# Performance work log

Hardware: AMD Instinct MI355X
Metric: run time of the kernel (lower is better)

Reference implementation:

```python
import jax, jax.numpy as jnp
import numpy as np

N_NODES = 100000
N_EDGES = 1600000
D_IN = 128
D_OUT = 5


def setup_inputs() -> dict:
    key = jax.random.key(0)
    k1, k2, k3, k4, k5 = jax.random.split(key, 5)
    x = jax.random.normal(k1, (N_NODES, D_IN), dtype=jnp.float32)
    edge_index = jax.random.randint(k2, (2, N_EDGES), 0, N_NODES, dtype=jnp.int64)
    scale = 1.0 / np.sqrt(D_IN)
    W_l = jax.random.normal(k3, (D_OUT, D_IN), dtype=jnp.float32) * scale
    b_l = jax.random.normal(k4, (D_OUT,), dtype=jnp.float32) * scale
    W_r = jax.random.normal(k5, (D_OUT, D_IN), dtype=jnp.float32) * scale
    return {"x": x, "edge_index": edge_index, "W_l": W_l, "b_l": b_l, "W_r": W_r}


def reference(x, edge_index, W_l, b_l, W_r):
    # PyG SAGEConv with aggr='mean', root_weight=True:
    # out_i = mean_{j: (j->i) in E} x_j @ W_l^T + b_l + x_i @ W_r^T
    n = x.shape[0]
    src = edge_index[0]
    dst = edge_index[1]
    msgs = x[src]  # [E, D_in] gather (irregular access)
    agg_sum = jax.ops.segment_sum(msgs, dst, num_segments=n)  # [N, D_in]
    deg = jax.ops.segment_sum(jnp.ones(src.shape, dtype=x.dtype), dst, num_segments=n)
    agg_mean = agg_sum / jnp.maximum(deg, 1.0)[:, None]  # zero-degree nodes -> 0
    out = agg_mean @ W_l.T + b_l + x @ W_r.T  # [N, D_out]
    return out
```

## Files before the change

kernel.cpp:

```cpp
#include <hip/hip_runtime.h>
#include <hip/hip_bf16.h>


#define N_NODES 100000
#define N_EDGES 1600000
#define D_IN 128

#define HL_STRIDE 8
#define N_PAD 100352

#define B_NODES 196
#define N_BUCKETS 512
#define CAP 3840

#define SC_EPT 8
#define SC_EPB (256 * SC_EPT)
#define SC_GRID ((N_EDGES + SC_EPB - 1) / SC_EPB)

#define NPG 8
#define PROJ_NPB (16 * NPG)
#define PROJ_BLOCKS ((N_NODES + PROJ_NPB - 1) / PROJ_NPB)
#define FUSED_GRID (PROJ_BLOCKS + SC_GRID)

#define FXS 262144.0f
#define FXB 16777216u
#define FXBF 16777216.0f
#define INV_FXS (1.0f / 262144.0f)

typedef unsigned long long u64;
typedef unsigned int u32;

__global__ __launch_bounds__(256, 4) void proj_scatter_kernel(
    const float* __restrict__ x,
    const float* __restrict__ Wl,
    const float* __restrict__ Wr,
    float* __restrict__ hl,
    float* __restrict__ hr,
    const int* __restrict__ ei,
    u32* __restrict__ sorted,
    int* __restrict__ cursor)
{
    const int tid = threadIdx.x;

    if (blockIdx.x < PROJ_BLOCKS) {
        const int g = tid >> 4;
        const int k = tid & 15;

        float4 wv[10][2];
#pragma unroll
        for (int o = 0; o < 10; ++o) {
            const float* w = (o < 5 ? Wl + o * D_IN : Wr + (o - 5) * D_IN) + k * 8;
            wv[o][0] = ((const float4*)w)[0];
            wv[o][1] = ((const float4*)w)[1];
        }

        const int node0 = blockIdx.x * PROJ_NPB + g * NPG;

#pragma unroll
        for (int it = 0; it < NPG; ++it) {
            const int node = min(node0 + it, N_NODES - 1);

            const float4* xr = (const float4*)(x + (size_t)node * D_IN + k * 8);
            float4 x0 = xr[0];
            float4 x1 = xr[1];

            float s[10];
#pragma unroll
            for (int o = 0; o < 10; ++o) {
                s[o] = x0.x * wv[o][0].x + x0.y * wv[o][0].y
                     + x0.z * wv[o][0].z + x0.w * wv[o][0].w
                     + x1.x * wv[o][1].x + x1.y * wv[o][1].y
                     + x1.z * wv[o][1].z + x1.w * wv[o][1].w;
            }

#pragma unroll
            for (int o = 0; o < 10; ++o) {
                s[o] += __shfl_xor(s[o], 8, 64);
                s[o] += __shfl_xor(s[o], 4, 64);
                s[o] += __shfl_xor(s[o], 2, 64);
                s[o] += __shfl_xor(s[o], 1, 64);
            }

            if (k == 0) {
                float* pl = hl + (size_t)node * HL_STRIDE;
                *(float4*)pl = make_float4(s[0], s[1], s[2], s[3]);
                pl[4] = s[4];
                float* pr = hr + (size_t)node * HL_STRIDE;
                *(float4*)pr = make_float4(s[5], s[6], s[7], s[8]);
                pr[4] = s[9];
            }
        }
    } else {
        __shared__ int hist[N_BUCKETS];
        __shared__ int basepos[N_BUCKETS];

        for (int i = tid; i < N_BUCKETS; i += 256) hist[i] = 0;
        __syncthreads();

        const int blk = blockIdx.x - PROJ_BLOCKS;
        const int e0  = blk * SC_EPB + tid * SC_EPT;

        int srcv[SC_EPT], dstv[SC_EPT], slot[SC_EPT];
        bool valid[SC_EPT];

        if (e0 + SC_EPT <= N_EDGES) {
            const int4* s4 = (const int4*)(ei + e0);
            const int4* d4 = (const int4*)(ei + N_EDGES + e0);
            int4 sa = s4[0], sb = s4[1], da = d4[0], db = d4[1];
            srcv[0]=sa.x; srcv[1]=sa.y; srcv[2]=sa.z; srcv[3]=sa.w;
            srcv[4]=sb.x; srcv[5]=sb.y; srcv[6]=sb.z; srcv[7]=sb.w;
            dstv[0]=da.x; dstv[1]=da.y; dstv[2]=da.z; dstv[3]=da.w;
            dstv[4]=db.x; dstv[5]=db.y; dstv[6]=db.z; dstv[7]=db.w;
#pragma unroll
            for (int q = 0; q < SC_EPT; ++q) valid[q] = true;
        } else {
#pragma unroll
            for (int q = 0; q < SC_EPT; ++q) {
                int e = e0 + q;
                valid[q] = (e < N_EDGES);
                srcv[q] = valid[q] ? ei[e] : 0;
                dstv[q] = valid[q] ? ei[N_EDGES + e] : 0;
            }
        }

#pragma unroll
        for (int q = 0; q < SC_EPT; ++q) {
            if (valid[q]) {
                unsigned b = (unsigned)dstv[q] / 196u;
                slot[q] = atomicAdd(&hist[b], 1);
            }
        }
        __syncthreads();

        for (int b = tid; b < N_BUCKETS; b += 256) {
            int c = hist[b];
            if (c > 0) basepos[b] = atomicAdd(&cursor[b], c);
        }
        __syncthreads();

#pragma unroll
        for (int q = 0; q < SC_EPT; ++q) {
            if (valid[q]) {
                unsigned b = (unsigned)dstv[q] / 196u;
                unsigned r = (unsigned)dstv[q] - b * 196u;
                sorted[(size_t)b * CAP + basepos[b] + slot[q]] =
                    (r << 17) | (unsigned)srcv[q];
            }
        }
    }
}

__global__ __launch_bounds__(512) void agg_kernel(
    const u32* __restrict__ sorted,
    const int* __restrict__ cursor,
    const float* __restrict__ hl,
    const float* __restrict__ hr,
    const float* __restrict__ bias,
    float* __restrict__ out)
{
    __shared__ u64 acc[B_NODES * 3];

    const int b   = blockIdx.x;
    const int tid = threadIdx.x;

    for (int i = tid; i < B_NODES * 3; i += 512) acc[i] = 0ull;
    __syncthreads();

    const int cnt = cursor[b];
    const u32* sp = sorted + (size_t)b * CAP;
    const int nvec = cnt >> 2;

#define EMIT(hh, ee, rr)                                                     \
    {                                                                        \
        u32 f0 = __float2uint_rn(fmaf((hh).x, FXS, FXBF));                   \
        u32 f1 = __float2uint_rn(fmaf((hh).y, FXS, FXBF));                   \
        u32 f2 = __float2uint_rn(fmaf((hh).z, FXS, FXBF));                   \
        u32 f3 = __float2uint_rn(fmaf((hh).w, FXS, FXBF));                   \
        u32 f4 = __float2uint_rn(fmaf((ee),   FXS, FXBF));                   \
        u64* a = acc + (rr) * 3;                                             \
        atomicAdd(&a[0], ((u64)f1 << 32) | f0);                              \
        atomicAdd(&a[1], ((u64)f3 << 32) | f2);                              \
        atomicAdd(&a[2], ((u64)f4 << 32) | 1u);                              \
    }

    for (int it = tid; it < nvec; it += 512) {
        uint4 v = ((const uint4*)sp)[it];
        int s0 = (int)(v.x & 0x1FFFFu), r0 = (int)(v.x >> 17);
        int s1 = (int)(v.y & 0x1FFFFu), r1 = (int)(v.y >> 17);
        int s2 = (int)(v.z & 0x1FFFFu), r2 = (int)(v.z >> 17);
        int s3 = (int)(v.w & 0x1FFFFu), r3 = (int)(v.w >> 17);

        const float* p0 = hl + (size_t)s0 * HL_STRIDE;
        const float* p1 = hl + (size_t)s1 * HL_STRIDE;
        const float* p2 = hl + (size_t)s2 * HL_STRIDE;
        const float* p3 = hl + (size_t)s3 * HL_STRIDE;
        float4 h0 = *(const float4*)p0; float e0 = p0[4];
        float4 h1 = *(const float4*)p1; float e1 = p1[4];
        float4 h2 = *(const float4*)p2; float e2 = p2[4];
        float4 h3 = *(const float4*)p3; float e3 = p3[4];

        EMIT(h0, e0, r0) EMIT(h1, e1, r1) EMIT(h2, e2, r2) EMIT(h3, e3, r3)
    }
    for (int i = (nvec << 2) + tid; i < cnt; i += 512) {
        u32 v = sp[i];
        int src = (int)(v & 0x1FFFFu);
        int r   = (int)(v >> 17);
        const float* p = hl + (size_t)src * HL_STRIDE;
        float4 h = *(const float4*)p;
        float  e = p[4];
        EMIT(h, e, r)
    }
#undef EMIT
    __syncthreads();

    const int nodebase = b * B_NODES;
    for (int n = tid; n < B_NODES; n += 512) {
        int node = nodebase + n;
        if (node >= N_NODES) continue;
        u64 w0 = acc[n * 3 + 0];
        u64 w1 = acc[n * 3 + 1];
        u64 w2 = acc[n * 3 + 2];
        u32 deg = (u32)(w2 & 0xFFFFFFFFu);
        u32 db  = deg * FXB;
        int i0 = (int)((u32)(w0 & 0xFFFFFFFFu) - db);
        int i1 = (int)((u32)(w0 >> 32)         - db);
        int i2 = (int)((u32)(w1 & 0xFFFFFFFFu) - db);
        int i3 = (int)((u32)(w1 >> 32)         - db);
        int i4 = (int)((u32)(w2 >> 32)         - db);

        float rec = INV_FXS / fmaxf((float)deg, 1.0f);
        const float* h = hr + (size_t)node * HL_STRIDE;
        float* o = out + (size_t)node * 5;
        o[0] = (float)i0 * rec + bias[0] + h[0];
        o[1] = (float)i1 * rec + bias[1] + h[1];
        o[2] = (float)i2 * rec + bias[2] + h[2];
        o[3] = (float)i3 * rec + bias[3] + h[3];
        o[4] = (float)i4 * rec + bias[4] + h[4];
    }
}

extern "C" void kernel_launch(void* const* d_in, const int* in_sizes, int n_in,
                              void* d_out, int out_size, void* d_ws, size_t ws_size,
                              hipStream_t stream) {
    const float* x    = (const float*)d_in[0];
    const int*   ei   = (const int*)d_in[1];
    const float* Wl   = (const float*)d_in[2];
    const float* bl   = (const float*)d_in[3];
    const float* Wr   = (const float*)d_in[4];
    float*       out  = (float*)d_out;

    float* hl     = (float*)d_ws;
    float* hr     = hl + (size_t)N_PAD * HL_STRIDE;
    u32*   sorted = (u32*)(hr + (size_t)N_PAD * HL_STRIDE);
    int*   cursor = (int*)(sorted + (size_t)N_BUCKETS * CAP);

    hipMemsetAsync(cursor, 0, N_BUCKETS * sizeof(int), stream);

    proj_scatter_kernel<<<FUSED_GRID, 256, 0, stream>>>(
        x, Wl, Wr, hl, hr, ei, sorted, cursor);

    agg_kernel<<<N_BUCKETS, 512, 0, stream>>>(sorted, cursor, hl, hr, bl, out);
}
```

Before: 130.9 us.

## Scatter larger edge chunks per block with two-pass histogram to cut global atomics

Each scatter block now handles 16384 edges instead of 2048. It does a histogram pass over destination buckets, then a second pass that re-reads the edges and assigns slots, so each block issues one global cursor atomic per bucket over a much larger batch. The scatter blocks are also placed before the projection blocks in the grid so the latency-bound scatter work is dispatched first. In exchange the edge arrays are read twice, there are far fewer scatter blocks and so less parallelism in that phase, and more shared-memory atomic contention per block.

Measured after the change: 140.3 us. 1.07x slower.

```diff
diff --git a/kernel.cpp b/kernel.cpp
--- a/kernel.cpp
+++ b/kernel.cpp
@@ -13,14 +13,14 @@
 #define N_BUCKETS 512
 #define CAP 3840
 
-#define SC_EPT 8
-#define SC_EPB (256 * SC_EPT)
+#define SC_EPB 16384
 #define SC_GRID ((N_EDGES + SC_EPB - 1) / SC_EPB)
+#define SC_CHUNKS (SC_EPB / 1024)
 
 #define NPG 8
 #define PROJ_NPB (16 * NPG)
 #define PROJ_BLOCKS ((N_NODES + PROJ_NPB - 1) / PROJ_NPB)
-#define FUSED_GRID (PROJ_BLOCKS + SC_GRID)
+#define FUSED_GRID (SC_GRID + PROJ_BLOCKS)
 
 #define FXS 262144.0f
 #define FXB 16777216u
@@ -42,7 +42,57 @@
 {
     const int tid = threadIdx.x;
 
-    if (blockIdx.x < PROJ_BLOCKS) {
+    if (blockIdx.x < SC_GRID) {
+        __shared__ int hist[N_BUCKETS];
+        __shared__ int basepos[N_BUCKETS];
+
+        for (int i = tid; i < N_BUCKETS; i += 256) hist[i] = 0;
+        __syncthreads();
+
+        const int e0 = blockIdx.x * SC_EPB;
+
+#pragma unroll
+        for (int c = 0; c < SC_CHUNKS; ++c) {
+            int e = e0 + (c << 10) + (tid << 2);
+            if (e < N_EDGES) {
+                int4 d4 = *(const int4*)(ei + N_EDGES + e);
+                atomicAdd(&hist[(unsigned)d4.x / 196u], 1);
+                atomicAdd(&hist[(unsigned)d4.y / 196u], 1);
+                atomicAdd(&hist[(unsigned)d4.z / 196u], 1);
+                atomicAdd(&hist[(unsigned)d4.w / 196u], 1);
+            }
+        }
+        __syncthreads();
+
+        for (int b = tid; b < N_BUCKETS; b += 256) {
+            int c = hist[b];
+            if (c > 0) basepos[b] = atomicAdd(&cursor[b], c);
+        }
+        __syncthreads();
+
+        for (int i = tid; i < N_BUCKETS; i += 256) hist[i] = 0;
+        __syncthreads();
+
+#pragma unroll
+        for (int c = 0; c < SC_CHUNKS; ++c) {
+            int e = e0 + (c << 10) + (tid << 2);
+            if (e < N_EDGES) {
+                int4 s4 = *(const int4*)(ei + e);
+                int4 d4 = *(const int4*)(ei + N_EDGES + e);
+                int sv[4] = { s4.x, s4.y, s4.z, s4.w };
+                int dv[4] = { d4.x, d4.y, d4.z, d4.w };
+#pragma unroll
+                for (int q = 0; q < 4; ++q) {
+                    unsigned b = (unsigned)dv[q] / 196u;
+                    unsigned r = (unsigned)dv[q] - b * 196u;
+                    int slot = atomicAdd(&hist[b], 1);
+                    sorted[(size_t)b * CAP + basepos[b] + slot] =
+                        (r << 17) | (unsigned)sv[q];
+                }
+            }
+        }
+    } else {
+        const int pblk = blockIdx.x - SC_GRID;
         const int g = tid >> 4;
         const int k = tid & 15;
 
@@ -54,7 +104,7 @@
             wv[o][1] = ((const float4*)w)[1];
         }
 
-        const int node0 = blockIdx.x * PROJ_NPB + g * NPG;
+        const int node0 = pblk * PROJ_NPB + g * NPG;
 
 #pragma unroll
         for (int it = 0; it < NPG; ++it) {
@@ -88,63 +138,6 @@
                 float* pr = hr + (size_t)node * HL_STRIDE;
                 *(float4*)pr = make_float4(s[5], s[6], s[7], s[8]);
                 pr[4] = s[9];
-            }
-        }
-    } else {
-        __shared__ int hist[N_BUCKETS];
-        __shared__ int basepos[N_BUCKETS];
-
-        for (int i = tid; i < N_BUCKETS; i += 256) hist[i] = 0;
-        __syncthreads();
-
-        const int blk = blockIdx.x - PROJ_BLOCKS;
-        const int e0  = blk * SC_EPB + tid * SC_EPT;
-
-        int srcv[SC_EPT], dstv[SC_EPT], slot[SC_EPT];
-        bool valid[SC_EPT];
-
-        if (e0 + SC_EPT <= N_EDGES) {
-            const int4* s4 = (const int4*)(ei + e0);
-            const int4* d4 = (const int4*)(ei + N_EDGES + e0);
-            int4 sa = s4[0], sb = s4[1], da = d4[0], db = d4[1];
-            srcv[0]=sa.x; srcv[1]=sa.y; srcv[2]=sa.z; srcv[3]=sa.w;
-            srcv[4]=sb.x; srcv[5]=sb.y; srcv[6]=sb.z; srcv[7]=sb.w;
-            dstv[0]=da.x; dstv[1]=da.y; dstv[2]=da.z; dstv[3]=da.w;
-            dstv[4]=db.x; dstv[5]=db.y; dstv[6]=db.z; dstv[7]=db.w;
-#pragma unroll
-            for (int q = 0; q < SC_EPT; ++q) valid[q] = true;
-        } else {
-#pragma unroll
-            for (int q = 0; q < SC_EPT; ++q) {
-                int e = e0 + q;
-                valid[q] = (e < N_EDGES);
-                srcv[q] = valid[q] ? ei[e] : 0;
-                dstv[q] = valid[q] ? ei[N_EDGES + e] : 0;
-            }
-        }
-
-#pragma unroll
-        for (int q = 0; q < SC_EPT; ++q) {
-            if (valid[q]) {
-                unsigned b = (unsigned)dstv[q] / 196u;
-                slot[q] = atomicAdd(&hist[b], 1);
-            }
-        }
-        __syncthreads();
-
-        for (int b = tid; b < N_BUCKETS; b += 256) {
-            int c = hist[b];
-            if (c > 0) basepos[b] = atomicAdd(&cursor[b], c);
-        }
-        __syncthreads();
-
-#pragma unroll
-        for (int q = 0; q < SC_EPT; ++q) {
-            if (valid[q]) {
-                unsigned b = (unsigned)dstv[q] / 196u;
-                unsigned r = (unsigned)dstv[q] - b * 196u;
-                sorted[(size_t)b * CAP + basepos[b] + slot[q]] =
-                    (r << 17) | (unsigned)srcv[q];
             }
         }
     }
```

## Compute node projections with bf16 MFMA tiles instead of FP32 dot products

Applied to the files above, without the earlier changes.

Replaces the per-node FP32 dot-product-plus-shuffle-reduction projection with a 16x16x32 bf16 MFMA: each wave handles a 16-node tile, x rows and the 10 weight rows are converted to bf16 and accumulated over 4 K-steps. This removes the shuffle reductions and most VALU work in the projection part of the fused kernel. It trades precision (bf16 inputs), and the tile count assumes N_NODES is divisible by 16.

Result: no change. 132.2 us (+1.0%).

```diff
diff --git a/kernel.cpp b/kernel.cpp
--- a/kernel.cpp
+++ b/kernel.cpp
@@ -17,9 +17,8 @@
 #define SC_EPB (256 * SC_EPT)
 #define SC_GRID ((N_EDGES + SC_EPB - 1) / SC_EPB)
 
-#define NPG 8
-#define PROJ_NPB (16 * NPG)
-#define PROJ_BLOCKS ((N_NODES + PROJ_NPB - 1) / PROJ_NPB)
+#define N_TILES (N_NODES / 16)
+#define PROJ_BLOCKS ((N_TILES + 3) / 4)
 #define FUSED_GRID (PROJ_BLOCKS + SC_GRID)
 
 #define FXS 262144.0f
@@ -29,6 +28,23 @@
 
 typedef unsigned long long u64;
 typedef unsigned int u32;
+typedef __attribute__((ext_vector_type(8))) short bf16x8;
+typedef __attribute__((ext_vector_type(4))) float f32x4;
+
+__device__ __forceinline__ u32 pack_bf16(float lo, float hi) {
+    u32 a = (__float_as_uint(lo) + 0x8000u) >> 16;
+    u32 b = (__float_as_uint(hi) + 0x8000u) & 0xFFFF0000u;
+    return a | b;
+}
+
+__device__ __forceinline__ bf16x8 pack8(float4 v0, float4 v1) {
+    union { u32 w[4]; bf16x8 v; } u;
+    u.w[0] = pack_bf16(v0.x, v0.y);
+    u.w[1] = pack_bf16(v0.z, v0.w);
+    u.w[2] = pack_bf16(v1.x, v1.y);
+    u.w[3] = pack_bf16(v1.z, v1.w);
+    return u.v;
+}
 
 __global__ __launch_bounds__(256, 4) void proj_scatter_kernel(
     const float* __restrict__ x,
@@ -43,51 +59,44 @@
     const int tid = threadIdx.x;
 
     if (blockIdx.x < PROJ_BLOCKS) {
-        const int g = tid >> 4;
-        const int k = tid & 15;
-
-        float4 wv[10][2];
-#pragma unroll
-        for (int o = 0; o < 10; ++o) {
-            const float* w = (o < 5 ? Wl + o * D_IN : Wr + (o - 5) * D_IN) + k * 8;
-            wv[o][0] = ((const float4*)w)[0];
-            wv[o][1] = ((const float4*)w)[1];
-        }
-
-        const int node0 = blockIdx.x * PROJ_NPB + g * NPG;
-
-#pragma unroll
-        for (int it = 0; it < NPG; ++it) {
-            const int node = min(node0 + it, N_NODES - 1);
-
-            const float4* xr = (const float4*)(x + (size_t)node * D_IN + k * 8);
-            float4 x0 = xr[0];
-            float4 x1 = xr[1];
-
-            float s[10];
-#pragma unroll
-            for (int o = 0; o < 10; ++o) {
-                s[o] = x0.x * wv[o][0].x + x0.y * wv[o][0].y
-                     + x0.z * wv[o][0].z + x0.w * wv[o][0].w
-                     + x1.x * wv[o][1].x + x1.y * wv[o][1].y
-                     + x1.z * wv[o][1].z + x1.w * wv[o][1].w;
-            }
-
-#pragma unroll
-            for (int o = 0; o < 10; ++o) {
-                s[o] += __shfl_xor(s[o], 8, 64);
-                s[o] += __shfl_xor(s[o], 4, 64);
-                s[o] += __shfl_xor(s[o], 2, 64);
-                s[o] += __shfl_xor(s[o], 1, 64);
-            }
-
-            if (k == 0) {
-                float* pl = hl + (size_t)node * HL_STRIDE;
-                *(float4*)pl = make_float4(s[0], s[1], s[2], s[3]);
-                pl[4] = s[4];
-                float* pr = hr + (size_t)node * HL_STRIDE;
-                *(float4*)pr = make_float4(s[5], s[6], s[7], s[8]);
-                pr[4] = s[9];
+        const int wv   = blockIdx.x * 4 + (tid >> 6);
+        const int tile = min(wv, N_TILES - 1);
+        const int lane = tid & 63;
+        const int n    = lane & 15;
+        const int quad = lane >> 4;
+        const int kb   = quad * 8;
+
+        bf16x8 wf[4];
+        const bool wvalid = (n < 10);
+        const float* wrow = (n < 5) ? (Wl + n * D_IN) : (Wr + (n - 5) * D_IN);
+#pragma unroll
+        for (int t = 0; t < 4; ++t) {
+            if (wvalid) {
+                const float4* wp = (const float4*)(wrow + t * 32 + kb);
+                wf[t] = pack8(wp[0], wp[1]);
+            } else {
+                union { u32 w[4]; bf16x8 v; } z; 
+                z.w[0] = z.w[1] = z.w[2] = z.w[3] = 0u;
+                wf[t] = z.v;
+            }
+        }
+
+        const float* xrow = x + ((size_t)tile * 16 + n) * D_IN;
+        f32x4 acc = {0.f, 0.f, 0.f, 0.f};
+#pragma unroll
+        for (int t = 0; t < 4; ++t) {
+            const float4* xp = (const float4*)(xrow + t * 32 + kb);
+            bf16x8 af = pack8(xp[0], xp[1]);
+            acc = __builtin_amdgcn_mfma_f32_16x16x32_bf16(af, wf[t], acc, 0, 0, 0);
+        }
+
+        if (wvalid) {
+#pragma unroll
+            for (int r = 0; r < 4; ++r) {
+                const int node = tile * 16 + quad * 4 + r;
+                float* p = (n < 5) ? (hl + (size_t)node * HL_STRIDE + n)
+                                   : (hr + (size_t)node * HL_STRIDE + (n - 5));
+                *p = acc[r];
             }
         }
     } else {
```
